# Performance work log

Measured on AMD Instinct MI355X. Metric: run time of the kernel, lower is better.

Reference implementation:

```python
import jax, jax.numpy as jnp
import numpy as np

B, T, D_MODEL = 256, 200, 2048
D_KEY, D_VAL = 128, 128


def setup_inputs() -> dict:
    key = jax.random.key(0)
    k_q, k_mask, k_wq, k_wk, k_wv = jax.random.split(key, 5)
    q = jax.random.normal(k_q, (B, T, D_MODEL), dtype=jnp.float32)
    pad_mask = jax.random.randint(k_mask, (B, 1, T), 0, 2, dtype=jnp.int32)
    # ensure key 0 is never padded so every causal row has >=1 valid key (no NaN softmax)
    pad_mask = pad_mask.at[:, :, 0].set(0)
    s = 1.0 / np.sqrt(D_MODEL)
    Wq = jax.random.normal(k_wq, (D_KEY, D_MODEL), dtype=jnp.float32) * s
    Wk = jax.random.normal(k_wk, (D_KEY, D_MODEL), dtype=jnp.float32) * s
    Wv = jax.random.normal(k_wv, (D_VAL, D_MODEL), dtype=jnp.float32) * s
    return {"q": q, "pad_mask": pad_mask, "Wq": Wq, "Wk": Wk, "Wv": Wv}


def reference(q, pad_mask, Wq, Wk, Wv):
    # self-attention: kv = q
    T_ = q.shape[1]
    C = q.shape[-1]  # note: original scales by d_model, not d_key
    Q = jnp.einsum('btc,kc->btk', q, Wq)   # [B,T,d_key]
    K = jnp.einsum('btc,kc->btk', q, Wk)   # [B,T,d_key]
    V = jnp.einsum('btc,vc->btv', q, Wv)   # [B,T,d_val]
    W = jnp.einsum('bqk,btk->bqt', Q, K) / jnp.sqrt(jnp.asarray(C, q.dtype))  # [B,T,T]
    tril = jnp.tril(jnp.ones((T_, T_), dtype=jnp.bool_))
    neg_inf = jnp.asarray(-jnp.inf, W.dtype)
    W = jnp.where(tril[None, :, :], W, neg_inf)          # causal mask
    W = jnp.where(pad_mask == 1, neg_inf, W)             # padding mask (broadcast [B,1,T])
    W = jax.nn.softmax(W, axis=-1)
    # dropout p=0.0 / eval mode -> identity
    return jnp.einsum('bqt,btv->bqv', W, V)              # [B,T,d_val]
```

## Files before the change

kernel.cpp:

```cpp
#include <hip/hip_runtime.h>

typedef __bf16 bf16x8 __attribute__((ext_vector_type(8)));
typedef __bf16 bf16x4 __attribute__((ext_vector_type(4)));
typedef float  f32x4  __attribute__((ext_vector_type(4)));

#define MFMA16(a,b,c) __builtin_amdgcn_mfma_f32_16x16x32_bf16((a),(b),(c),0,0,0)

constexpr int B_ = 256, T_ = 200, DM = 2048, DK = 128;
constexpr int VT_STRIDE = 208;

constexpr size_t OFF_W = 0;
constexpr size_t OFF_Q = 1572864;
constexpr size_t OFF_K = OFF_Q + 13107200;
constexpr size_t OFF_V = OFF_K + 13107200;

#define GLOAD_LDS16(G, L)                                                     \
  __builtin_amdgcn_global_load_lds(                                           \
      (const __attribute__((address_space(1))) void*)(G),                     \
      (__attribute__((address_space(3))) void*)(L), 16, 0, 0)

__global__ __launch_bounds__(256) void wconv_kernel(const float* __restrict__ Wq,
                                                    const float* __restrict__ Wk,
                                                    const float* __restrict__ Wv,
                                                    __bf16* __restrict__ Wcat) {
  int idx = (blockIdx.x * 256 + threadIdx.x) * 4;
  int sel = idx >> 18;
  const float* base = (sel == 0) ? Wq : (sel == 1) ? Wk : Wv;
  float4 f = *(const float4*)(base + (idx - (sel << 18)));
  bf16x4 o;
  o[0] = (__bf16)f.x; o[1] = (__bf16)f.y; o[2] = (__bf16)f.z; o[3] = (__bf16)f.w;
  *(bf16x4*)(Wcat + idx) = o;
}

__global__ __launch_bounds__(256) void proj_kernel(const float* __restrict__ q,
                                                   const __bf16* __restrict__ Wcat,
                                                   __bf16* __restrict__ Qo,
                                                   __bf16* __restrict__ Ko,
                                                   __bf16* __restrict__ Vt) {
  __shared__ alignas(16) char smem[32768];

  const int tid  = threadIdx.x;
  const int lane = tid & 63;
  const int w    = tid >> 6;
  const int wm   = w >> 1, wn = w & 1;
  const int lhi  = lane >> 4, llo = lane & 15;

  const int d  = blockIdx.x;
  const int jj = (d & 7) * 150 + (d >> 3);
  const int mp = jj / 3, nb = jj - mp * 3;
  const int m0 = mp * 128;
  const int col0 = nb * 128;

  f32x4 acc[4][4];
#pragma unroll
  for (int i = 0; i < 4; ++i)
#pragma unroll
    for (int j = 0; j < 4; ++j) acc[i][j] = {0.f, 0.f, 0.f, 0.f};

  const int arow = tid >> 1, ahalf = tid & 1;
  const float* aptr = q + (size_t)(m0 + arow) * DM + ahalf * 16;
  const int aswz = (tid >> 2) & 3;
  const int aw0 = arow * 64 + (((ahalf * 2)     ^ aswz) << 4);
  const int aw1 = arow * 64 + (((ahalf * 2 + 1) ^ aswz) << 4);
  const __bf16* bgbase = Wcat + (size_t)(col0 + (tid >> 2)) * DM
                              + (((tid & 3) ^ ((tid >> 3) & 3)) << 3);
  const int fswz = (llo >> 1) & 3;
  const int aro  = (wm * 64 + llo) * 64 + ((lhi ^ fswz) << 4);
  const int bro  = (wn * 64 + llo) * 64 + ((lhi ^ fswz) << 4);

  f32x4 r0a, r0b, r0c, r0d, r1a, r1b, r1c, r1d;

#define A_ISSUE(RA, RB, RC, RD, K0)                                           \
  { const float* p_ = aptr + (K0);                                            \
    RA = *(const f32x4*)(p_);      RB = *(const f32x4*)(p_ + 4);              \
    RC = *(const f32x4*)(p_ + 8);  RD = *(const f32x4*)(p_ + 12); }

#define B_ISSUE(BUFB, K0)                                                     \
  { char* lb_ = smem + 8192 + (BUFB) * 16384 + tid * 16;                      \
    GLOAD_LDS16(bgbase + (K0), lb_);                                          \
    GLOAD_LDS16(bgbase + (size_t)64 * DM + (K0), lb_ + 4096); }

#define A_PUB(RA, RB, RC, RD, BUFB)                                           \
  { char* la_ = smem + (BUFB) * 16384;                                        \
    bf16x8 p0, p1;                                                            \
    p0[0]=(__bf16)RA[0]; p0[1]=(__bf16)RA[1]; p0[2]=(__bf16)RA[2]; p0[3]=(__bf16)RA[3]; \
    p0[4]=(__bf16)RB[0]; p0[5]=(__bf16)RB[1]; p0[6]=(__bf16)RB[2]; p0[7]=(__bf16)RB[3]; \
    p1[0]=(__bf16)RC[0]; p1[1]=(__bf16)RC[1]; p1[2]=(__bf16)RC[2]; p1[3]=(__bf16)RC[3]; \
    p1[4]=(__bf16)RD[0]; p1[5]=(__bf16)RD[1]; p1[6]=(__bf16)RD[2]; p1[7]=(__bf16)RD[3]; \
    *(bf16x8*)(la_ + aw0) = p0;                                               \
    *(bf16x8*)(la_ + aw1) = p1; }

#define COMPUTE(BUFB)                                                         \
  { const char* la_ = smem + (BUFB) * 16384;                                  \
    const char* lb_ = la_ + 8192;                                             \
    bf16x8 af[4], bfr[4];                                                     \
    _Pragma("unroll")                                                         \
    for (int i = 0; i < 4; ++i) af[i]  = *(const bf16x8*)(la_ + aro + i * 1024); \
    _Pragma("unroll")                                                         \
    for (int j = 0; j < 4; ++j) bfr[j] = *(const bf16x8*)(lb_ + bro + j * 1024); \
    _Pragma("unroll")                                                         \
    for (int i = 0; i < 4; ++i)                                               \
      _Pragma("unroll")                                                       \
      for (int j = 0; j < 4; ++j) acc[i][j] = MFMA16(af[i], bfr[j], acc[i][j]); }

#define VMW(N)  asm volatile("s_waitcnt vmcnt(" #N ")" ::: "memory")
#define LGKM0() asm volatile("s_waitcnt lgkmcnt(0)" ::: "memory")
#define BAR()   __builtin_amdgcn_s_barrier()

  constexpr int NK = DM / 32;
  A_ISSUE(r0a, r0b, r0c, r0d, 0);
  A_ISSUE(r1a, r1b, r1c, r1d, 32);
  B_ISSUE(0, 0);
  A_PUB(r0a, r0b, r0c, r0d, 0);
  VMW(0);
  LGKM0();
  BAR();

  for (int tp = 0; tp < 31; ++tp) {
    const int t0 = tp * 2;
    {
      B_ISSUE(1, (t0 + 1) * 32);
      A_ISSUE(r0a, r0b, r0c, r0d, (t0 + 2) * 32);
      VMW(10);
      BAR();
      COMPUTE(0);
      A_PUB(r1a, r1b, r1c, r1d, 1);
      LGKM0();
      BAR();
    }
    {
      B_ISSUE(0, (t0 + 2) * 32);
      A_ISSUE(r1a, r1b, r1c, r1d, (t0 + 3) * 32);
      VMW(10);
      BAR();
      COMPUTE(1);
      A_PUB(r0a, r0b, r0c, r0d, 0);
      LGKM0();
      BAR();
    }
  }
  {
    B_ISSUE(1, 63 * 32);
    VMW(6);
    BAR();
    COMPUTE(0);
    A_PUB(r1a, r1b, r1c, r1d, 1);
    LGKM0();
    BAR();
  }
  {
    VMW(0);
    BAR();
    COMPUTE(1);
  }
#undef A_ISSUE
#undef B_ISSUE
#undef A_PUB
#undef COMPUTE
#undef VMW
#undef LGKM0
#undef BAR

  if (nb == 0) {
#pragma unroll
    for (int i = 0; i < 4; ++i)
#pragma unroll
      for (int r = 0; r < 4; ++r) {
        int row = m0 + wm * 64 + i * 16 + lhi * 4 + r;
#pragma unroll
        for (int j = 0; j < 4; ++j)
          Qo[(size_t)row * DK + wn * 64 + j * 16 + llo] = (__bf16)acc[i][j][r];
      }
  } else if (nb == 1) {
#pragma unroll
    for (int i = 0; i < 4; ++i)
#pragma unroll
      for (int r = 0; r < 4; ++r) {
        int row = m0 + wm * 64 + i * 16 + lhi * 4 + r;
#pragma unroll
        for (int j = 0; j < 4; ++j)
          Ko[(size_t)row * DK + wn * 64 + j * 16 + llo] = (__bf16)acc[i][j][r];
      }
  } else {
#pragma unroll
    for (int i = 0; i < 4; ++i)
#pragma unroll
      for (int r = 0; r < 4; ++r) {
        int row = m0 + wm * 64 + i * 16 + lhi * 4 + r;
        int b = row / 200;
        int t = row - b * 200;
#pragma unroll
        for (int j = 0; j < 4; ++j) {
          int col = wn * 64 + j * 16 + llo;
          Vt[((size_t)b * DK + col) * VT_STRIDE + t] = (__bf16)acc[i][j][r];
        }
      }
  }
}

template <int QB>
__global__ __launch_bounds__(256, 1) void attn_kernel(const __bf16* __restrict__ Qg,
                                                      const __bf16* __restrict__ Kg,
                                                      const __bf16* __restrict__ Vt,
                                                      const int* __restrict__ padm,
                                                      float* __restrict__ out) {
  constexpr int Q0     = QB * 64;
  constexpr int KMAX   = (Q0 + 64 < T_) ? (Q0 + 64) : T_;
  constexpr int KTILES = (KMAX + 15) / 16;
  constexpr int KCC    = (KMAX + 31) / 32;
  constexpr int KT16   = KTILES * 16;
  constexpr int KP     = KCC * 32;
  constexpr int VS     = KP + 8;

  __shared__ __bf16 sK[KT16][136];
  __shared__ __bf16 sV[128][VS];
  __shared__ __bf16 sP[4][16][VS];
  __shared__ float  sMask[KT16];

  const int tid  = threadIdx.x;
  const int lane = tid & 63;
  const int w    = tid >> 6;
  const int b    = blockIdx.x;
  const int lhi  = lane >> 4, llo = lane & 15;

  for (int t = tid; t < KT16; t += 256) {
    float mv = -1e30f;
    if (t < KMAX && padm[b * T_ + t] == 0) mv = 0.0f;
    sMask[t] = mv;
  }
  for (int cid = tid; cid < KT16 * 16; cid += 256) {
    int t = cid >> 4, c = (cid & 15) * 8;
    int tg = (t < T_) ? t : (T_ - 1);
    *(bf16x8*)&sK[t][c] = *(const bf16x8*)(Kg + ((size_t)b * T_ + tg) * DK + c);
  }
  {
    constexpr int NCH = KP / 8;
    for (int cid = tid; cid < 128 * NCH; cid += 256) {
      int v = cid / NCH, t0 = (cid % NCH) * 8;
      bf16x8 val;
      if (t0 < VT_STRIDE) {
        val = *(const bf16x8*)(Vt + ((size_t)b * DK + v) * VT_STRIDE + t0);
      } else {
#pragma unroll
        for (int jz = 0; jz < 8; ++jz) val[jz] = (__bf16)0.0f;
      }
      *(bf16x8*)&sV[v][t0] = val;
    }
  }
  if constexpr (KT16 < KP) {
    constexpr int NC = (KP - KT16) / 8;
    for (int idx = tid; idx < 4 * 16 * NC; idx += 256) {
      int ww = idx / (16 * NC);
      int rem = idx % (16 * NC);
      int row = rem / NC, cc = (rem % NC) * 8;
      bf16x8 z;
#pragma unroll
      for (int jz = 0; jz < 8; ++jz) z[jz] = (__bf16)0.0f;
      *(bf16x8*)&sP[ww][row][KT16 + cc] = z;
    }
  }
  __syncthreads();

  const int q0w = Q0 + w * 16;
  bf16x8 qf[4];
  {
    int qrow = q0w + llo;
    if (qrow > T_ - 1) qrow = T_ - 1;
    const __bf16* qp = Qg + ((size_t)b * T_ + qrow) * DK + lhi * 8;
#pragma unroll
    for (int kk = 0; kk < 4; ++kk) qf[kk] = *(const bf16x8*)(qp + kk * 32);
  }

  float sc[KTILES][4];
  const float scale = 0.022097086912079608f;
#pragma unroll
  for (int tt = 0; tt < KTILES; ++tt) {
    f32x4 s = {0.f, 0.f, 0.f, 0.f};
    const __bf16* kp = &sK[tt * 16 + llo][lhi * 8];
#pragma unroll
    for (int kk = 0; kk < 4; ++kk) {
      bf16x8 kf = *(const bf16x8*)(kp + kk * 32);
      s = MFMA16(qf[kk], kf, s);
    }
    const int t = tt * 16 + llo;
    const float madd = sMask[t];
#pragma unroll
    for (int r = 0; r < 4; ++r) {
      int qq = q0w + lhi * 4 + r;
      float v = fmaf(s[r], scale, madd);
      sc[tt][r] = (t > qq) ? -1e30f : v;
    }
  }

#pragma unroll
  for (int r = 0; r < 4; ++r) {
    float mm = -3e38f;
#pragma unroll
    for (int tt = 0; tt < KTILES; ++tt) mm = fmaxf(mm, sc[tt][r]);
#pragma unroll
    for (int off = 1; off < 16; off <<= 1) mm = fmaxf(mm, __shfl_xor(mm, off));
    float ss = 0.f;
#pragma unroll
    for (int tt = 0; tt < KTILES; ++tt) { float e = __expf(sc[tt][r] - mm); sc[tt][r] = e; ss += e; }
#pragma unroll
    for (int off = 1; off < 16; off <<= 1) ss += __shfl_xor(ss, off);
    float inv = 1.0f / ss;
#pragma unroll
    for (int tt = 0; tt < KTILES; ++tt) sc[tt][r] *= inv;
  }

#pragma unroll
  for (int tt = 0; tt < KTILES; ++tt) {
    int t = tt * 16 + llo;
#pragma unroll
    for (int r = 0; r < 4; ++r) sP[w][lhi * 4 + r][t] = (__bf16)sc[tt][r];
  }
  __syncthreads();

  f32x4 oacc[8];
#pragma unroll
  for (int vt = 0; vt < 8; ++vt) oacc[vt] = {0.f, 0.f, 0.f, 0.f};
#pragma unroll
  for (int kc = 0; kc < KCC; ++kc) {
    bf16x8 pa = *(const bf16x8*)&sP[w][llo][kc * 32 + lhi * 8];
#pragma unroll
    for (int vt = 0; vt < 8; ++vt) {
      bf16x8 vb = *(const bf16x8*)&sV[vt * 16 + llo][kc * 32 + lhi * 8];
      oacc[vt] = MFMA16(pa, vb, oacc[vt]);
    }
  }

#pragma unroll
  for (int vt = 0; vt < 8; ++vt) {
#pragma unroll
    for (int r = 0; r < 4; ++r) {
      int qq = q0w + lhi * 4 + r;
      if (qq < T_) out[((size_t)b * T_ + qq) * DK + vt * 16 + llo] = oacc[vt][r];
    }
  }
}

extern "C" void kernel_launch(void* const* d_in, const int* in_sizes, int n_in,
                              void* d_out, int out_size, void* d_ws, size_t ws_size,
                              hipStream_t stream) {
  const float* q    = (const float*)d_in[0];
  const int*   padm = (const int*)d_in[1];
  const float* Wq   = (const float*)d_in[2];
  const float* Wk   = (const float*)d_in[3];
  const float* Wv   = (const float*)d_in[4];
  float* out        = (float*)d_out;

  char* ws = (char*)d_ws;
  __bf16* Wcat = (__bf16*)(ws + OFF_W);
  __bf16* Qb   = (__bf16*)(ws + OFF_Q);
  __bf16* Kb   = (__bf16*)(ws + OFF_K);
  __bf16* Vtb  = (__bf16*)(ws + OFF_V);

  wconv_kernel<<<768, 256, 0, stream>>>(Wq, Wk, Wv, Wcat);
  proj_kernel<<<1200, 256, 0, stream>>>(q, Wcat, Qb, Kb, Vtb);
  attn_kernel<0><<<256, 256, 0, stream>>>(Qb, Kb, Vtb, padm, out);
  attn_kernel<1><<<256, 256, 0, stream>>>(Qb, Kb, Vtb, padm, out);
  attn_kernel<2><<<256, 256, 0, stream>>>(Qb, Kb, Vtb, padm, out);
  attn_kernel<3><<<256, 256, 0, stream>>>(Qb, Kb, Vtb, padm, out);
}
```

Before: 279.9 us.

## Deepen QKV GEMM A-prefetch to three register stages, one barrier per step

```diff
diff --git a/kernel.cpp b/kernel.cpp
--- a/kernel.cpp
+++ b/kernel.cpp
@@ -68,7 +68,7 @@
   const int aro  = (wm * 64 + llo) * 64 + ((lhi ^ fswz) << 4);
   const int bro  = (wn * 64 + llo) * 64 + ((lhi ^ fswz) << 4);
 
-  f32x4 r0a, r0b, r0c, r0d, r1a, r1b, r1c, r1d;
+  f32x4 s0a, s0b, s0c, s0d, s1a, s1b, s1c, s1d, s2a, s2b, s2c, s2d;
 
 #define A_ISSUE(RA, RB, RC, RD, K0)                                           \
   { const float* p_ = aptr + (K0);                                            \
@@ -103,54 +103,62 @@
       _Pragma("unroll")                                                       \
       for (int j = 0; j < 4; ++j) acc[i][j] = MFMA16(af[i], bfr[j], acc[i][j]); }
 
-#define VMW(N)  asm volatile("s_waitcnt vmcnt(" #N ")" ::: "memory")
-#define LGKM0() asm volatile("s_waitcnt lgkmcnt(0)" ::: "memory")
-#define BAR()   __builtin_amdgcn_s_barrier()
-
-  constexpr int NK = DM / 32;
-  A_ISSUE(r0a, r0b, r0c, r0d, 0);
-  A_ISSUE(r1a, r1b, r1c, r1d, 32);
+#define VMW(N)   asm volatile("s_waitcnt vmcnt(" #N ")" ::: "memory")
+#define LGKM0()  asm volatile("s_waitcnt lgkmcnt(0)" ::: "memory")
+#define BARF()   { __builtin_amdgcn_s_barrier(); asm volatile("" ::: "memory"); }
+#define SCHED0() __builtin_amdgcn_sched_barrier(0)
+
+#define BODY(BUF, PA, PB, PC, PD, IA, IB, IC, ID, T)                          \
+  {                                                                           \
+    VMW(4);                                                                   \
+    BARF();                                                                   \
+    B_ISSUE((BUF) ^ 1, ((T) + 1) * 32);                                       \
+    A_ISSUE(IA, IB, IC, ID, ((T) + 3) * 32);                                  \
+    COMPUTE(BUF);                                                             \
+    SCHED0();                                                                 \
+    A_PUB(PA, PB, PC, PD, (BUF) ^ 1);                                         \
+    LGKM0();                                                                  \
+  }
+
+  A_ISSUE(s0a, s0b, s0c, s0d, 0);
+  A_ISSUE(s1a, s1b, s1c, s1d, 32);
+  A_ISSUE(s2a, s2b, s2c, s2d, 64);
   B_ISSUE(0, 0);
-  A_PUB(r0a, r0b, r0c, r0d, 0);
+  A_PUB(s0a, s0b, s0c, s0d, 0);
   VMW(0);
   LGKM0();
-  BAR();
-
-  for (int tp = 0; tp < 31; ++tp) {
-    const int t0 = tp * 2;
-    {
-      B_ISSUE(1, (t0 + 1) * 32);
-      A_ISSUE(r0a, r0b, r0c, r0d, (t0 + 2) * 32);
-      VMW(10);
-      BAR();
-      COMPUTE(0);
-      A_PUB(r1a, r1b, r1c, r1d, 1);
-      LGKM0();
-      BAR();
-    }
-    {
-      B_ISSUE(0, (t0 + 2) * 32);
-      A_ISSUE(r1a, r1b, r1c, r1d, (t0 + 3) * 32);
-      VMW(10);
-      BAR();
-      COMPUTE(1);
-      A_PUB(r0a, r0b, r0c, r0d, 0);
-      LGKM0();
-      BAR();
-    }
-  }
-  {
+
+  for (int tp = 0; tp < 10; ++tp) {
+    const int t0 = tp * 6;
+    BODY(0, s1a,s1b,s1c,s1d, s0a,s0b,s0c,s0d, t0 + 0);
+    BODY(1, s2a,s2b,s2c,s2d, s1a,s1b,s1c,s1d, t0 + 1);
+    BODY(0, s0a,s0b,s0c,s0d, s2a,s2b,s2c,s2d, t0 + 2);
+    BODY(1, s1a,s1b,s1c,s1d, s0a,s0b,s0c,s0d, t0 + 3);
+    BODY(0, s2a,s2b,s2c,s2d, s1a,s1b,s1c,s1d, t0 + 4);
+    BODY(1, s0a,s0b,s0c,s0d, s2a,s2b,s2c,s2d, t0 + 5);
+  }
+  BODY(0, s1a,s1b,s1c,s1d, s0a,s0b,s0c,s0d, 60);
+  {
+    VMW(4);
+    BARF();
+    B_ISSUE(0, 62 * 32);
+    COMPUTE(1);
+    SCHED0();
+    A_PUB(s2a, s2b, s2c, s2d, 0);
+    LGKM0();
+  }
+  {
+    VMW(0);
+    BARF();
     B_ISSUE(1, 63 * 32);
-    VMW(6);
-    BAR();
     COMPUTE(0);
-    A_PUB(r1a, r1b, r1c, r1d, 1);
+    SCHED0();
+    A_PUB(s0a, s0b, s0c, s0d, 1);
     LGKM0();
-    BAR();
   }
   {
     VMW(0);
-    BAR();
+    BARF();
     COMPUTE(1);
   }
 #undef A_ISSUE
@@ -159,7 +167,9 @@
 #undef COMPUTE
 #undef VMW
 #undef LGKM0
-#undef BAR
+#undef BARF
+#undef SCHED0
+#undef BODY
 
   if (nb == 0) {
 #pragma unroll
```

Measured after the change: 260.8 us. -6.8%, faster.

## Load projection B fragments directly to registers, halve LDS, raise occupancy

Applied to the files above, without the earlier changes.

```diff
diff --git a/kernel.cpp b/kernel.cpp
--- a/kernel.cpp
+++ b/kernel.cpp
@@ -13,11 +13,6 @@
 constexpr size_t OFF_Q = 1572864;
 constexpr size_t OFF_K = OFF_Q + 13107200;
 constexpr size_t OFF_V = OFF_K + 13107200;
-
-#define GLOAD_LDS16(G, L)                                                     \
-  __builtin_amdgcn_global_load_lds(                                           \
-      (const __attribute__((address_space(1))) void*)(G),                     \
-      (__attribute__((address_space(3))) void*)(L), 16, 0, 0)
 
 __global__ __launch_bounds__(256) void wconv_kernel(const float* __restrict__ Wq,
                                                     const float* __restrict__ Wk,
@@ -32,12 +27,12 @@
   *(bf16x4*)(Wcat + idx) = o;
 }
 
-__global__ __launch_bounds__(256) void proj_kernel(const float* __restrict__ q,
-                                                   const __bf16* __restrict__ Wcat,
-                                                   __bf16* __restrict__ Qo,
-                                                   __bf16* __restrict__ Ko,
-                                                   __bf16* __restrict__ Vt) {
-  __shared__ alignas(16) char smem[32768];
+__global__ __launch_bounds__(256, 3) void proj_kernel(const float* __restrict__ q,
+                                                      const __bf16* __restrict__ Wcat,
+                                                      __bf16* __restrict__ Qo,
+                                                      __bf16* __restrict__ Ko,
+                                                      __bf16* __restrict__ Vt) {
+  __shared__ alignas(16) char smem[16384];
 
   const int tid  = threadIdx.x;
   const int lane = tid & 63;
@@ -59,29 +54,31 @@
 
   const int arow = tid >> 1, ahalf = tid & 1;
   const float* aptr = q + (size_t)(m0 + arow) * DM + ahalf * 16;
-  const int aswz = (tid >> 2) & 3;
+  const int aswz = (arow & 3) ^ ((arow >> 2) & 3);
   const int aw0 = arow * 64 + (((ahalf * 2)     ^ aswz) << 4);
   const int aw1 = arow * 64 + (((ahalf * 2 + 1) ^ aswz) << 4);
-  const __bf16* bgbase = Wcat + (size_t)(col0 + (tid >> 2)) * DM
-                              + (((tid & 3) ^ ((tid >> 3) & 3)) << 3);
-  const int fswz = (llo >> 1) & 3;
+  const int fswz = (llo & 3) ^ ((llo >> 2) & 3);
   const int aro  = (wm * 64 + llo) * 64 + ((lhi ^ fswz) << 4);
-  const int bro  = (wn * 64 + llo) * 64 + ((lhi ^ fswz) << 4);
-
-  f32x4 r0a, r0b, r0c, r0d, r1a, r1b, r1c, r1d;
-
-#define A_ISSUE(RA, RB, RC, RD, K0)                                           \
-  { const float* p_ = aptr + (K0);                                            \
+
+  const __bf16* bptr = Wcat + (size_t)(col0 + wn * 64 + llo) * DM + lhi * 8;
+
+  f32x4 sA0a, sA0b, sA0c, sA0d, sA1a, sA1b, sA1c, sA1d;
+  bf16x8 b0f0, b0f1, b0f2, b0f3, b1f0, b1f1, b1f2, b1f3;
+
+#define A_ISSUE(RA, RB, RC, RD, T)                                            \
+  { const float* p_ = aptr + (T) * 32;                                        \
     RA = *(const f32x4*)(p_);      RB = *(const f32x4*)(p_ + 4);              \
     RC = *(const f32x4*)(p_ + 8);  RD = *(const f32x4*)(p_ + 12); }
 
-#define B_ISSUE(BUFB, K0)                                                     \
-  { char* lb_ = smem + 8192 + (BUFB) * 16384 + tid * 16;                      \
-    GLOAD_LDS16(bgbase + (K0), lb_);                                          \
-    GLOAD_LDS16(bgbase + (size_t)64 * DM + (K0), lb_ + 4096); }
-
-#define A_PUB(RA, RB, RC, RD, BUFB)                                           \
-  { char* la_ = smem + (BUFB) * 16384;                                        \
+#define B_LOAD(F0, F1, F2, F3, T)                                             \
+  { const __bf16* p_ = bptr + (size_t)(T) * 32;                               \
+    F0 = *(const bf16x8*)(p_);                                                \
+    F1 = *(const bf16x8*)(p_ + (size_t)16 * DM);                              \
+    F2 = *(const bf16x8*)(p_ + (size_t)32 * DM);                              \
+    F3 = *(const bf16x8*)(p_ + (size_t)48 * DM); }
+
+#define A_PUB(RA, RB, RC, RD, BUF)                                            \
+  { char* la_ = smem + (BUF) * 8192;                                          \
     bf16x8 p0, p1;                                                            \
     p0[0]=(__bf16)RA[0]; p0[1]=(__bf16)RA[1]; p0[2]=(__bf16)RA[2]; p0[3]=(__bf16)RA[3]; \
     p0[4]=(__bf16)RB[0]; p0[5]=(__bf16)RB[1]; p0[6]=(__bf16)RB[2]; p0[7]=(__bf16)RB[3]; \
@@ -90,74 +87,78 @@
     *(bf16x8*)(la_ + aw0) = p0;                                               \
     *(bf16x8*)(la_ + aw1) = p1; }
 
-#define COMPUTE(BUFB)                                                         \
-  { const char* la_ = smem + (BUFB) * 16384;                                  \
-    const char* lb_ = la_ + 8192;                                             \
-    bf16x8 af[4], bfr[4];                                                     \
+#define COMPUTE(BUF, F0, F1, F2, F3)                                          \
+  { const char* la_ = smem + (BUF) * 8192;                                    \
+    bf16x8 af[4];                                                             \
     _Pragma("unroll")                                                         \
-    for (int i = 0; i < 4; ++i) af[i]  = *(const bf16x8*)(la_ + aro + i * 1024); \
+    for (int i = 0; i < 4; ++i) af[i] = *(const bf16x8*)(la_ + aro + i * 1024); \
     _Pragma("unroll")                                                         \
-    for (int j = 0; j < 4; ++j) bfr[j] = *(const bf16x8*)(lb_ + bro + j * 1024); \
-    _Pragma("unroll")                                                         \
-    for (int i = 0; i < 4; ++i)                                               \
-      _Pragma("unroll")                                                       \
-      for (int j = 0; j < 4; ++j) acc[i][j] = MFMA16(af[i], bfr[j], acc[i][j]); }
-
-#define VMW(N)  asm volatile("s_waitcnt vmcnt(" #N ")" ::: "memory")
+    for (int i = 0; i < 4; ++i) {                                             \
+      acc[i][0] = MFMA16(af[i], F0, acc[i][0]);                               \
+      acc[i][1] = MFMA16(af[i], F1, acc[i][1]);                               \
+      acc[i][2] = MFMA16(af[i], F2, acc[i][2]);                               \
+      acc[i][3] = MFMA16(af[i], F3, acc[i][3]);                               \
+    } }
+
 #define LGKM0() asm volatile("s_waitcnt lgkmcnt(0)" ::: "memory")
-#define BAR()   __builtin_amdgcn_s_barrier()
-
-  constexpr int NK = DM / 32;
-  A_ISSUE(r0a, r0b, r0c, r0d, 0);
-  A_ISSUE(r1a, r1b, r1c, r1d, 32);
-  B_ISSUE(0, 0);
-  A_PUB(r0a, r0b, r0c, r0d, 0);
-  VMW(0);
+#define BAR()   { __builtin_amdgcn_s_barrier(); asm volatile("" ::: "memory"); }
+
+  A_ISSUE(sA0a, sA0b, sA0c, sA0d, 0);
+  B_LOAD(b0f0, b0f1, b0f2, b0f3, 0);
+  A_ISSUE(sA1a, sA1b, sA1c, sA1d, 1);
+  A_PUB(sA0a, sA0b, sA0c, sA0d, 0);
   LGKM0();
   BAR();
 
-  for (int tp = 0; tp < 31; ++tp) {
-    const int t0 = tp * 2;
+  for (int tp = 0; tp < 30; ++tp) {
+    const int u = tp * 2;
     {
-      B_ISSUE(1, (t0 + 1) * 32);
-      A_ISSUE(r0a, r0b, r0c, r0d, (t0 + 2) * 32);
-      VMW(10);
-      BAR();
-      COMPUTE(0);
-      A_PUB(r1a, r1b, r1c, r1d, 1);
+      B_LOAD(b1f0, b1f1, b1f2, b1f3, u + 1);
+      A_ISSUE(sA0a, sA0b, sA0c, sA0d, u + 2);
+      COMPUTE(0, b0f0, b0f1, b0f2, b0f3);
+      A_PUB(sA1a, sA1b, sA1c, sA1d, 1);
       LGKM0();
       BAR();
     }
     {
-      B_ISSUE(0, (t0 + 2) * 32);
-      A_ISSUE(r1a, r1b, r1c, r1d, (t0 + 3) * 32);
-      VMW(10);
-      BAR();
-      COMPUTE(1);
-      A_PUB(r0a, r0b, r0c, r0d, 0);
+      B_LOAD(b0f0, b0f1, b0f2, b0f3, u + 2);
+      A_ISSUE(sA1a, sA1b, sA1c, sA1d, u + 3);
+      COMPUTE(1, b1f0, b1f1, b1f2, b1f3);
+      A_PUB(sA0a, sA0b, sA0c, sA0d, 0);
       LGKM0();
       BAR();
     }
   }
   {
-    B_ISSUE(1, 63 * 32);
-    VMW(6);
-    BAR();
-    COMPUTE(0);
-    A_PUB(r1a, r1b, r1c, r1d, 1);
+    B_LOAD(b1f0, b1f1, b1f2, b1f3, 61);
+    A_ISSUE(sA0a, sA0b, sA0c, sA0d, 62);
+    COMPUTE(0, b0f0, b0f1, b0f2, b0f3);
+    A_PUB(sA1a, sA1b, sA1c, sA1d, 1);
     LGKM0();
     BAR();
   }
   {
-    VMW(0);
+    B_LOAD(b0f0, b0f1, b0f2, b0f3, 62);
+    A_ISSUE(sA1a, sA1b, sA1c, sA1d, 63);
+    COMPUTE(1, b1f0, b1f1, b1f2, b1f3);
+    A_PUB(sA0a, sA0b, sA0c, sA0d, 0);
+    LGKM0();
     BAR();
-    COMPUTE(1);
+  }
+  {
+    B_LOAD(b1f0, b1f1, b1f2, b1f3, 63);
+    COMPUTE(0, b0f0, b0f1, b0f2, b0f3);
+    A_PUB(sA1a, sA1b, sA1c, sA1d, 1);
+    LGKM0();
+    BAR();
+  }
+  {
+    COMPUTE(1, b1f0, b1f1, b1f2, b1f3);
   }
 #undef A_ISSUE
-#undef B_ISSUE
+#undef B_LOAD
 #undef A_PUB
 #undef COMPUTE
-#undef VMW
 #undef LGKM0
 #undef BAR
 
```

New measurement: 332.9 us. 1.19x slower.
